# Kernel tuning notes

Hardware: AMD Instinct MI355X
Metric: run time of the kernel (lower is better)

Reference implementation:

```python
import jax, jax.numpy as jnp
import numpy as np

TOPK_RATIO = 0.2
DICE_WEIGHT = 0.5
SHAPE = (2, 1, 128, 192, 192)


def setup_inputs() -> dict:
    key = jax.random.key(0)
    k1, k2 = jax.random.split(key)
    logits = jax.random.normal(k1, SHAPE, dtype=jnp.float32)
    targets = jax.random.uniform(k2, SHAPE, dtype=jnp.float32)
    return {"logits": logits, "targets": targets}


def _bce_with_logits(x, t):
    # stable: max(x,0) - x*t + log(1+exp(-|x|))
    return jnp.maximum(x, 0.0) - x * t + jnp.log1p(jnp.exp(-jnp.abs(x)))


def reference(logits, targets):
    # --- TopK BCE ---
    flat_loss = _bce_with_logits(logits, targets).reshape(-1)
    n = flat_loss.shape[0]
    k_samples = max(1, int(n * TOPK_RATIO))
    topk_losses, _ = jax.lax.top_k(flat_loss, k_samples)
    bce = jnp.mean(topk_losses)

    # --- Soft Dice ---
    p = jax.nn.sigmoid(logits).reshape(-1)
    t = targets.reshape(-1)
    intersection = jnp.sum(p * t)
    union = jnp.sum(p) + jnp.sum(t)
    dice = (2.0 * intersection + 1e-06) / (union + 1e-06)
    dice_loss = 1.0 - dice

    return bce + DICE_WEIGHT * dice_loss
```

## Files before the change

### kernel.cpp

```cpp
#include <hip/hip_runtime.h>
#include <math.h>
#include <limits.h>

#define NB1 8192
#define NB2 4096
#define VEC 4

__device__ __forceinline__ void elem_f(float x, float t, float& l, float& p) {
    float e = __expf(-fabsf(x));
    l = fmaxf(x, 0.f) - x * t + __logf(1.f + e);
    float r = __builtin_amdgcn_rcpf(1.f + e);
    p = (x >= 0.f) ? r : e * r;
}

__global__ __launch_bounds__(256) void sample_kernel(
    const float4* __restrict__ x4, const float4* __restrict__ t4,
    unsigned* __restrict__ H1, int n4)
{
    __shared__ unsigned lh[NB1];
    for (int i = threadIdx.x; i < NB1; i += 256) lh[i] = 0u;
    __syncthreads();

    int nth = gridDim.x * 256;
    int tid = blockIdx.x * 256 + threadIdx.x;
    int S4 = n4 >> 4;
    int i0 = tid, i1 = tid + nth;

    float4 xa, ta, xb, tb;
    bool v0 = i0 < S4, v1 = i1 < S4;
    if (v0) {
        int f4 = ((i0 >> 6) << 10) + (i0 & 63);
        xa = x4[f4]; ta = t4[f4];
    }
    if (v1) {
        int f4 = ((i1 >> 6) << 10) + (i1 & 63);
        xb = x4[f4]; tb = t4[f4];
    }
    if (v0) {
        float xs[4] = {xa.x, xa.y, xa.z, xa.w};
        float ts[4] = {ta.x, ta.y, ta.z, ta.w};
        #pragma unroll
        for (int c = 0; c < 4; ++c) {
            float l, p; elem_f(xs[c], ts[c], l, p);
            atomicAdd(&lh[__float_as_uint(l) >> 19], 1u);
        }
    }
    if (v1) {
        float xs[4] = {xb.x, xb.y, xb.z, xb.w};
        float ts[4] = {tb.x, tb.y, tb.z, tb.w};
        #pragma unroll
        for (int c = 0; c < 4; ++c) {
            float l, p; elem_f(xs[c], ts[c], l, p);
            atomicAdd(&lh[__float_as_uint(l) >> 19], 1u);
        }
    }
    __syncthreads();
    for (int i = threadIdx.x; i < NB1; i += 256) {
        unsigned c = lh[i];
        if (c) atomicAdd(&H1[i], c);
    }
}

__global__ __launch_bounds__(256) void band_kernel(
    const unsigned* __restrict__ H1, float* __restrict__ band,
    long long ks, long long M)
{
    __shared__ unsigned lh[NB1];
    const uint4* hv = (const uint4*)H1;
    uint4* lv = (uint4*)lh;
    for (int i = threadIdx.x; i < NB1 / 4; i += 256) lv[i] = hv[i];
    __syncthreads();
    if (threadIdx.x >= 64) return;

    int lane = threadIdx.x;
    int base = lane << 7;
    unsigned long long chunk = 0;
    for (int j = 0; j < 128; ++j) chunk += lh[base + j];
    unsigned long long s = chunk;
    #pragma unroll
    for (int off = 1; off < 64; off <<= 1) {
        unsigned long long v = __shfl_down(s, off);
        if (lane + off < 64) s += v;
    }
    unsigned long long above = s - chunk;

    int my_bhi = INT_MAX, my_blo = -1;
    unsigned long long c = above;
    for (int j = 127; j >= 0; --j) {
        unsigned h = lh[base + j];
        if ((long long)(c + h) < ks - M) my_bhi = base + j;
        if ((long long)c > ks + M && my_blo < 0) my_blo = base + j;
        c += h;
    }
    #pragma unroll
    for (int off = 32; off; off >>= 1) {
        int a = __shfl_down(my_bhi, off); my_bhi = min(my_bhi, a);
        int b = __shfl_down(my_blo, off); my_blo = max(my_blo, b);
    }
    if (lane == 0) {
        int bhi = (my_bhi == INT_MAX) ? (NB1 - 1) : my_bhi;
        int blo = my_blo;
        float vhi = __uint_as_float((unsigned)bhi << 19);
        float vlo = (blo < 0) ? 0.f : __uint_as_float((unsigned)(blo + 1) << 19);
        if (!(vlo < vhi)) vlo = 0.f;
        band[0] = vlo;
        band[1] = vhi;
    }
}

__device__ __forceinline__ void process4(
    float4 xv, float4 tv, float vlo, float vhi, float scale,
    float& sp, float& spt, float& st, float& sgt, unsigned& cnt,
    unsigned* __restrict__ hist2)
{
    float xs[4] = {xv.x, xv.y, xv.z, xv.w};
    float ts[4] = {tv.x, tv.y, tv.z, tv.w};
    #pragma unroll
    for (int c = 0; c < 4; ++c) {
        float l, p;
        elem_f(xs[c], ts[c], l, p);
        sp += p; spt += p * ts[c]; st += ts[c];
        if (l >= vhi) { cnt++; sgt += l; }
        else if (l >= vlo) {
            int b = min((int)((l - vlo) * scale), NB2 - 1);
            atomicAdd(&hist2[b], 1u);
        }
    }
}

__global__ __launch_bounds__(256, 4) void main_kernel(
    const float4* __restrict__ x4, const float4* __restrict__ t4,
    const float* __restrict__ band, unsigned* __restrict__ hist2,
    float* __restrict__ q0, float* __restrict__ q1,
    float* __restrict__ q2, float* __restrict__ q3, unsigned* __restrict__ qc,
    const float* __restrict__ xg, const float* __restrict__ tg,
    int n, int n4)
{
    float vlo = band[0], vhi = band[1];
    float scale = (float)NB2 / (vhi - vlo);

    int base = blockIdx.x * (256 * VEC) + threadIdx.x;
    float sp = 0.f, spt = 0.f, st = 0.f, sgt = 0.f;
    unsigned cnt = 0;

    bool full = (blockIdx.x + 1) * (256 * VEC) <= n4;
    if (full) {
        float4 xv[VEC], tv[VEC];
        #pragma unroll
        for (int j = 0; j < VEC; ++j) xv[j] = x4[base + j * 256];
        #pragma unroll
        for (int j = 0; j < VEC; ++j) tv[j] = t4[base + j * 256];
        #pragma unroll
        for (int j = 0; j < VEC; ++j)
            process4(xv[j], tv[j], vlo, vhi, scale, sp, spt, st, sgt, cnt, hist2);
    } else {
        for (int j = 0; j < VEC; ++j) {
            int idx = base + j * 256;
            if (idx < n4)
                process4(x4[idx], t4[idx], vlo, vhi, scale, sp, spt, st, sgt, cnt, hist2);
        }
    }
    int tail0 = n4 << 2;
    if (blockIdx.x == 0 && threadIdx.x < (n - tail0)) {
        float x = xg[tail0 + threadIdx.x], t = tg[tail0 + threadIdx.x];
        float l, p;
        elem_f(x, t, l, p);
        sp += p; spt += p * t; st += t;
        if (l >= vhi) { cnt++; sgt += l; }
        else if (l >= vlo) {
            int b = min((int)((l - vlo) * scale), NB2 - 1);
            atomicAdd(&hist2[b], 1u);
        }
    }

    #pragma unroll
    for (int off = 32; off; off >>= 1) {
        sp  += __shfl_down(sp,  off);
        spt += __shfl_down(spt, off);
        st  += __shfl_down(st,  off);
        sgt += __shfl_down(sgt, off);
        cnt += __shfl_down(cnt, off);
    }
    __shared__ float    rs[4][4];
    __shared__ unsigned rc[4];
    int w = threadIdx.x >> 6;
    if ((threadIdx.x & 63) == 0) {
        rs[w][0] = sp; rs[w][1] = spt; rs[w][2] = st; rs[w][3] = sgt; rc[w] = cnt;
    }
    __syncthreads();
    if (threadIdx.x == 0) {
        float a0 = 0, a1 = 0, a2 = 0, a3 = 0;
        unsigned c = 0;
        #pragma unroll
        for (int i = 0; i < 4; ++i) {
            a0 += rs[i][0]; a1 += rs[i][1]; a2 += rs[i][2]; a3 += rs[i][3]; c += rc[i];
        }
        q0[blockIdx.x] = a0; q1[blockIdx.x] = a1; q2[blockIdx.x] = a2;
        q3[blockIdx.x] = a3; qc[blockIdx.x] = c;
    }
}

__global__ __launch_bounds__(1024) void final_kernel(
    const unsigned* __restrict__ hist2, const float* __restrict__ band,
    const float* __restrict__ q0, const float* __restrict__ q1,
    const float* __restrict__ q2, const float* __restrict__ q3,
    const unsigned* __restrict__ qc, int nblocks,
    float* __restrict__ out, long long k)
{
    __shared__ unsigned lh[NB2];
    __shared__ double red[16][5];
    __shared__ double fin[5];

    for (int i = threadIdx.x; i < NB2; i += 1024) lh[i] = hist2[i];

    double a0 = 0, a1 = 0, a2 = 0, a3 = 0, a4 = 0;
    for (int i = threadIdx.x; i < nblocks; i += 1024) {
        a0 += (double)q0[i]; a1 += (double)q1[i]; a2 += (double)q2[i];
        a3 += (double)q3[i]; a4 += (double)qc[i];
    }
    #pragma unroll
    for (int off = 32; off; off >>= 1) {
        a0 += __shfl_down(a0, off); a1 += __shfl_down(a1, off);
        a2 += __shfl_down(a2, off); a3 += __shfl_down(a3, off);
        a4 += __shfl_down(a4, off);
    }
    int w = threadIdx.x >> 6;
    if ((threadIdx.x & 63) == 0) {
        red[w][0] = a0; red[w][1] = a1; red[w][2] = a2; red[w][3] = a3; red[w][4] = a4;
    }
    __syncthreads();
    if (threadIdx.x == 0) {
        double f0 = 0, f1 = 0, f2 = 0, f3 = 0, f4 = 0;
        for (int i = 0; i < 16; ++i) {
            f0 += red[i][0]; f1 += red[i][1]; f2 += red[i][2];
            f3 += red[i][3]; f4 += red[i][4];
        }
        fin[0] = f0; fin[1] = f1; fin[2] = f2; fin[3] = f3; fin[4] = f4;
    }
    __syncthreads();
    if (threadIdx.x >= 64) return;

    int lane = threadIdx.x;
    double SP = fin[0], SPT = fin[1], ST = fin[2], SGT = fin[3];
    long long CNT = (long long)fin[4];

    double vlo = (double)band[0], vhi = (double)band[1];
    double binw = (vhi - vlo) / NB2;
    long long k2 = k - CNT;

    int base = lane << 6;
    unsigned long long cchunk = 0;
    double wchunk = 0.0;
    for (int j = 0; j < 64; ++j) {
        unsigned h = lh[base + j];
        cchunk += h;
        wchunk += (double)h * (vlo + (base + j + 0.5) * binw);
    }
    unsigned long long cs = cchunk;
    double wsum = wchunk;
    #pragma unroll
    for (int off = 1; off < 64; off <<= 1) {
        unsigned long long cv = __shfl_down(cs, off);
        double wv = __shfl_down(wsum, off);
        if (lane + off < 64) { cs += cv; wsum += wv; }
    }
    unsigned long long total = __shfl(cs, 0);
    double wtotal = __shfl(wsum, 0);

    double I = SPT, U = SP + ST;
    double dice_part = 0.5 * (1.0 - (2.0 * I + 1e-6) / (U + 1e-6));

    if (k2 <= 0) {
        if (lane == 0) out[0] = (float)(SGT / (double)k + dice_part);
        return;
    }
    if ((unsigned long long)k2 > total) {
        if (lane == 0) {
            double sum_top = SGT + wtotal + (double)(k2 - (long long)total) * vlo;
            out[0] = (float)(sum_top / (double)k + dice_part);
        }
        return;
    }
    unsigned long long c = cs - cchunk;
    double wacc = wsum - wchunk;
    for (int j = 63; j >= 0; --j) {
        unsigned h = lh[base + j];
        double val = vlo + (base + j + 0.5) * binw;
        if (c < (unsigned long long)k2 && (unsigned long long)k2 <= c + h) {
            double sum_top = SGT + wacc + (double)((long long)k2 - (long long)c) * val;
            out[0] = (float)(sum_top / (double)k + dice_part);
        }
        c += h;
        wacc += (double)h * val;
    }
}

extern "C" void kernel_launch(void* const* d_in, const int* in_sizes, int n_in,
                              void* d_out, int out_size, void* d_ws, size_t ws_size,
                              hipStream_t stream)
{
    const float* x = (const float*)d_in[0];
    const float* t = (const float*)d_in[1];
    float* out = (float*)d_out;
    int n = in_sizes[0];
    int n4 = n >> 2;
    long long k = (long long)((double)n * 0.2);
    if (k < 1) k = 1;

    long long S = (long long)(n4 >> 4) * 4;
    long long ks = (S > 0) ? (long long)((double)k * (double)S / (double)n) : 0;
    long long M = 4096;

    int tilesz = 256 * VEC;
    int grid = (n4 + tilesz - 1) / tilesz;
    if (grid < 1) grid = 1;

    int S4 = n4 >> 4;
    int sgrid = (S4 + 511) / 512;
    if (sgrid < 1) sgrid = 1;

    unsigned char* ws = (unsigned char*)d_ws;
    unsigned* H1    = (unsigned*)(ws);
    unsigned* hist2 = (unsigned*)(ws + 32768);
    float*    band  = (float*)(ws + 49152);
    size_t po = 50176;
    size_t pstride = (((size_t)grid * 4) + 255) & ~(size_t)255;
    float*    q0 = (float*)(ws + po);
    float*    q1 = (float*)(ws + po + pstride);
    float*    q2 = (float*)(ws + po + 2 * pstride);
    float*    q3 = (float*)(ws + po + 3 * pstride);
    unsigned* qc = (unsigned*)(ws + po + 4 * pstride);

    hipMemsetAsync(d_ws, 0, 49152, stream);

    sample_kernel<<<sgrid, 256, 0, stream>>>((const float4*)x, (const float4*)t, H1, n4);
    band_kernel<<<1, 256, 0, stream>>>(H1, band, ks, M);
    main_kernel<<<grid, 256, 0, stream>>>((const float4*)x, (const float4*)t,
                                          band, hist2, q0, q1, q2, q3, qc, x, t, n, n4);
    final_kernel<<<1, 1024, 0, stream>>>(hist2, band, q0, q1, q2, q3, qc, grid, out, k);
}
```

Before: 137.6 us.

## Fuse band and final stages into preceding kernels via last-block pattern

Replaces the four-kernel pipeline and memset with two kernels. The last block to finish, detected with a global atomic counter and threadfence, does the band selection and the final top-k and dice reduction. Histograms and counters move to __device__ globals that the last block resets for the next call. This removes two launches and a memset, but adds fence and atomic work to every block and a 16KB shared buffer to the main kernel, which may lower occupancy.

```diff
diff --git a/kernel.cpp b/kernel.cpp
--- a/kernel.cpp
+++ b/kernel.cpp
@@ -5,6 +5,12 @@
 #define NB1 8192
 #define NB2 4096
 #define VEC 4
+
+__device__ unsigned g_H1[NB1];
+__device__ unsigned g_hist2[NB2];
+__device__ float    g_band[2];
+__device__ unsigned g_done1 = 0;
+__device__ unsigned g_done2 = 0;
 
 __device__ __forceinline__ void elem_f(float x, float t, float& l, float& p) {
     float e = __expf(-fabsf(x));
@@ -13,11 +19,12 @@
     p = (x >= 0.f) ? r : e * r;
 }
 
-__global__ __launch_bounds__(256) void sample_kernel(
+__global__ __launch_bounds__(256) void sample_band_kernel(
     const float4* __restrict__ x4, const float4* __restrict__ t4,
-    unsigned* __restrict__ H1, int n4)
+    int n4, long long ks, long long M)
 {
     __shared__ unsigned lh[NB1];
+    __shared__ int is_last;
     for (int i = threadIdx.x; i < NB1; i += 256) lh[i] = 0u;
     __syncthreads();
 
@@ -57,54 +64,60 @@
     __syncthreads();
     for (int i = threadIdx.x; i < NB1; i += 256) {
         unsigned c = lh[i];
-        if (c) atomicAdd(&H1[i], c);
-    }
-}
-
-__global__ __launch_bounds__(256) void band_kernel(
-    const unsigned* __restrict__ H1, float* __restrict__ band,
-    long long ks, long long M)
-{
-    __shared__ unsigned lh[NB1];
-    const uint4* hv = (const uint4*)H1;
+        if (c) atomicAdd(&g_H1[i], c);
+    }
+    __syncthreads();
+
+    if (threadIdx.x == 0) {
+        __threadfence();
+        is_last = (atomicAdd(&g_done1, 1u) == (unsigned)(gridDim.x - 1));
+    }
+    __syncthreads();
+    if (!is_last) return;
+    __threadfence();
+
+    const uint4* hv = (const uint4*)g_H1;
     uint4* lv = (uint4*)lh;
     for (int i = threadIdx.x; i < NB1 / 4; i += 256) lv[i] = hv[i];
     __syncthreads();
-    if (threadIdx.x >= 64) return;
-
-    int lane = threadIdx.x;
-    int base = lane << 7;
-    unsigned long long chunk = 0;
-    for (int j = 0; j < 128; ++j) chunk += lh[base + j];
-    unsigned long long s = chunk;
-    #pragma unroll
-    for (int off = 1; off < 64; off <<= 1) {
-        unsigned long long v = __shfl_down(s, off);
-        if (lane + off < 64) s += v;
-    }
-    unsigned long long above = s - chunk;
-
-    int my_bhi = INT_MAX, my_blo = -1;
-    unsigned long long c = above;
-    for (int j = 127; j >= 0; --j) {
-        unsigned h = lh[base + j];
-        if ((long long)(c + h) < ks - M) my_bhi = base + j;
-        if ((long long)c > ks + M && my_blo < 0) my_blo = base + j;
-        c += h;
-    }
-    #pragma unroll
-    for (int off = 32; off; off >>= 1) {
-        int a = __shfl_down(my_bhi, off); my_bhi = min(my_bhi, a);
-        int b = __shfl_down(my_blo, off); my_blo = max(my_blo, b);
-    }
-    if (lane == 0) {
-        int bhi = (my_bhi == INT_MAX) ? (NB1 - 1) : my_bhi;
-        int blo = my_blo;
-        float vhi = __uint_as_float((unsigned)bhi << 19);
-        float vlo = (blo < 0) ? 0.f : __uint_as_float((unsigned)(blo + 1) << 19);
-        if (!(vlo < vhi)) vlo = 0.f;
-        band[0] = vlo;
-        band[1] = vhi;
+    for (int i = threadIdx.x; i < NB1; i += 256) g_H1[i] = 0u;
+    if (threadIdx.x == 0) g_done1 = 0u;
+
+    if (threadIdx.x < 64) {
+        int lane = threadIdx.x;
+        int base = lane << 7;
+        unsigned long long chunk = 0;
+        for (int j = 0; j < 128; ++j) chunk += lh[base + j];
+        unsigned long long s = chunk;
+        #pragma unroll
+        for (int off = 1; off < 64; off <<= 1) {
+            unsigned long long v = __shfl_down(s, off);
+            if (lane + off < 64) s += v;
+        }
+        unsigned long long above = s - chunk;
+
+        int my_bhi = INT_MAX, my_blo = -1;
+        unsigned long long c = above;
+        for (int j = 127; j >= 0; --j) {
+            unsigned h = lh[base + j];
+            if ((long long)(c + h) < ks - M) my_bhi = base + j;
+            if ((long long)c > ks + M && my_blo < 0) my_blo = base + j;
+            c += h;
+        }
+        #pragma unroll
+        for (int off = 32; off; off >>= 1) {
+            int a = __shfl_down(my_bhi, off); my_bhi = min(my_bhi, a);
+            int b = __shfl_down(my_blo, off); my_blo = max(my_blo, b);
+        }
+        if (lane == 0) {
+            int bhi = (my_bhi == INT_MAX) ? (NB1 - 1) : my_bhi;
+            int blo = my_blo;
+            float vhi = __uint_as_float((unsigned)bhi << 19);
+            float vlo = (blo < 0) ? 0.f : __uint_as_float((unsigned)(blo + 1) << 19);
+            if (!(vlo < vhi)) vlo = 0.f;
+            g_band[0] = vlo;
+            g_band[1] = vhi;
+        }
     }
 }
 
@@ -128,15 +141,21 @@
     }
 }
 
-__global__ __launch_bounds__(256, 4) void main_kernel(
+__global__ __launch_bounds__(256, 4) void main_final_kernel(
     const float4* __restrict__ x4, const float4* __restrict__ t4,
-    const float* __restrict__ band, unsigned* __restrict__ hist2,
     float* __restrict__ q0, float* __restrict__ q1,
     float* __restrict__ q2, float* __restrict__ q3, unsigned* __restrict__ qc,
     const float* __restrict__ xg, const float* __restrict__ tg,
-    int n, int n4)
+    int n, int n4, float* __restrict__ out, long long k)
 {
-    float vlo = band[0], vhi = band[1];
+    __shared__ float    rs[4][4];
+    __shared__ unsigned rc[4];
+    __shared__ int      is_last;
+    __shared__ unsigned lh2[NB2];
+    __shared__ double   red[4][5];
+    __shared__ double   fin[5];
+
+    float vlo = g_band[0], vhi = g_band[1];
     float scale = (float)NB2 / (vhi - vlo);
 
     int base = blockIdx.x * (256 * VEC) + threadIdx.x;
@@ -152,12 +171,12 @@
         for (int j = 0; j < VEC; ++j) tv[j] = t4[base + j * 256];
         #pragma unroll
         for (int j = 0; j < VEC; ++j)
-            process4(xv[j], tv[j], vlo, vhi, scale, sp, spt, st, sgt, cnt, hist2);
+            process4(xv[j], tv[j], vlo, vhi, scale, sp, spt, st, sgt, cnt, g_hist2);
     } else {
         for (int j = 0; j < VEC; ++j) {
             int idx = base + j * 256;
             if (idx < n4)
-                process4(x4[idx], t4[idx], vlo, vhi, scale, sp, spt, st, sgt, cnt, hist2);
+                process4(x4[idx], t4[idx], vlo, vhi, scale, sp, spt, st, sgt, cnt, g_hist2);
         }
     }
     int tail0 = n4 << 2;
@@ -169,7 +188,7 @@
         if (l >= vhi) { cnt++; sgt += l; }
         else if (l >= vlo) {
             int b = min((int)((l - vlo) * scale), NB2 - 1);
-            atomicAdd(&hist2[b], 1u);
+            atomicAdd(&g_hist2[b], 1u);
         }
     }
 
@@ -181,8 +200,6 @@
         sgt += __shfl_down(sgt, off);
         cnt += __shfl_down(cnt, off);
     }
-    __shared__ float    rs[4][4];
-    __shared__ unsigned rc[4];
     int w = threadIdx.x >> 6;
     if ((threadIdx.x & 63) == 0) {
         rs[w][0] = sp; rs[w][1] = spt; rs[w][2] = st; rs[w][3] = sgt; rc[w] = cnt;
@@ -197,24 +214,18 @@
         }
         q0[blockIdx.x] = a0; q1[blockIdx.x] = a1; q2[blockIdx.x] = a2;
         q3[blockIdx.x] = a3; qc[blockIdx.x] = c;
-    }
-}
-
-__global__ __launch_bounds__(1024) void final_kernel(
-    const unsigned* __restrict__ hist2, const float* __restrict__ band,
-    const float* __restrict__ q0, const float* __restrict__ q1,
-    const float* __restrict__ q2, const float* __restrict__ q3,
-    const unsigned* __restrict__ qc, int nblocks,
-    float* __restrict__ out, long long k)
-{
-    __shared__ unsigned lh[NB2];
-    __shared__ double red[16][5];
-    __shared__ double fin[5];
-
-    for (int i = threadIdx.x; i < NB2; i += 1024) lh[i] = hist2[i];
+        __threadfence();
+        is_last = (atomicAdd(&g_done2, 1u) == (unsigned)(gridDim.x - 1));
+    }
+    __syncthreads();
+    if (!is_last) return;
+    __threadfence();
+
+    int nblocks = gridDim.x;
+    for (int i = threadIdx.x; i < NB2; i += 256) lh2[i] = g_hist2[i];
 
     double a0 = 0, a1 = 0, a2 = 0, a3 = 0, a4 = 0;
-    for (int i = threadIdx.x; i < nblocks; i += 1024) {
+    for (int i = threadIdx.x; i < nblocks; i += 256) {
         a0 += (double)q0[i]; a1 += (double)q1[i]; a2 += (double)q2[i];
         a3 += (double)q3[i]; a4 += (double)qc[i];
     }
@@ -224,74 +235,75 @@
         a2 += __shfl_down(a2, off); a3 += __shfl_down(a3, off);
         a4 += __shfl_down(a4, off);
     }
-    int w = threadIdx.x >> 6;
+    int w2 = threadIdx.x >> 6;
     if ((threadIdx.x & 63) == 0) {
-        red[w][0] = a0; red[w][1] = a1; red[w][2] = a2; red[w][3] = a3; red[w][4] = a4;
+        red[w2][0] = a0; red[w2][1] = a1; red[w2][2] = a2; red[w2][3] = a3; red[w2][4] = a4;
     }
     __syncthreads();
     if (threadIdx.x == 0) {
         double f0 = 0, f1 = 0, f2 = 0, f3 = 0, f4 = 0;
-        for (int i = 0; i < 16; ++i) {
+        for (int i = 0; i < 4; ++i) {
             f0 += red[i][0]; f1 += red[i][1]; f2 += red[i][2];
             f3 += red[i][3]; f4 += red[i][4];
         }
         fin[0] = f0; fin[1] = f1; fin[2] = f2; fin[3] = f3; fin[4] = f4;
-    }
-    __syncthreads();
-    if (threadIdx.x >= 64) return;
-
-    int lane = threadIdx.x;
-    double SP = fin[0], SPT = fin[1], ST = fin[2], SGT = fin[3];
-    long long CNT = (long long)fin[4];
-
-    double vlo = (double)band[0], vhi = (double)band[1];
-    double binw = (vhi - vlo) / NB2;
-    long long k2 = k - CNT;
-
-    int base = lane << 6;
-    unsigned long long cchunk = 0;
-    double wchunk = 0.0;
-    for (int j = 0; j < 64; ++j) {
-        unsigned h = lh[base + j];
-        cchunk += h;
-        wchunk += (double)h * (vlo + (base + j + 0.5) * binw);
-    }
-    unsigned long long cs = cchunk;
-    double wsum = wchunk;
-    #pragma unroll
-    for (int off = 1; off < 64; off <<= 1) {
-        unsigned long long cv = __shfl_down(cs, off);
-        double wv = __shfl_down(wsum, off);
-        if (lane + off < 64) { cs += cv; wsum += wv; }
-    }
-    unsigned long long total = __shfl(cs, 0);
-    double wtotal = __shfl(wsum, 0);
-
-    double I = SPT, U = SP + ST;
-    double dice_part = 0.5 * (1.0 - (2.0 * I + 1e-6) / (U + 1e-6));
-
-    if (k2 <= 0) {
-        if (lane == 0) out[0] = (float)(SGT / (double)k + dice_part);
-        return;
-    }
-    if ((unsigned long long)k2 > total) {
-        if (lane == 0) {
-            double sum_top = SGT + wtotal + (double)(k2 - (long long)total) * vlo;
-            out[0] = (float)(sum_top / (double)k + dice_part);
-        }
-        return;
-    }
-    unsigned long long c = cs - cchunk;
-    double wacc = wsum - wchunk;
-    for (int j = 63; j >= 0; --j) {
-        unsigned h = lh[base + j];
-        double val = vlo + (base + j + 0.5) * binw;
-        if (c < (unsigned long long)k2 && (unsigned long long)k2 <= c + h) {
-            double sum_top = SGT + wacc + (double)((long long)k2 - (long long)c) * val;
-            out[0] = (float)(sum_top / (double)k + dice_part);
-        }
-        c += h;
-        wacc += (double)h * val;
+        g_done2 = 0u;
+    }
+    __syncthreads();
+    for (int i = threadIdx.x; i < NB2; i += 256) g_hist2[i] = 0u;
+
+    if (threadIdx.x < 64) {
+        int lane = threadIdx.x;
+        double SP = fin[0], SPT = fin[1], ST = fin[2], SGT = fin[3];
+        long long CNT = (long long)fin[4];
+
+        double dvlo = (double)vlo, dvhi = (double)vhi;
+        double binw = (dvhi - dvlo) / NB2;
+        long long k2 = k - CNT;
+
+        int base2 = lane << 6;
+        unsigned long long cchunk = 0;
+        double wchunk = 0.0;
+        for (int j = 0; j < 64; ++j) {
+            unsigned h = lh2[base2 + j];
+            cchunk += h;
+            wchunk += (double)h * (dvlo + (base2 + j + 0.5) * binw);
+        }
+        unsigned long long cs = cchunk;
+        double wsum = wchunk;
+        #pragma unroll
+        for (int off = 1; off < 64; off <<= 1) {
+            unsigned long long cv = __shfl_down(cs, off);
+            double wv = __shfl_down(wsum, off);
+            if (lane + off < 64) { cs += cv; wsum += wv; }
+        }
+        unsigned long long total = __shfl(cs, 0);
+        double wtotal = __shfl(wsum, 0);
+
+        double I = SPT, U = SP + ST;
+        double dice_part = 0.5 * (1.0 - (2.0 * I + 1e-6) / (U + 1e-6));
+
+        if (k2 <= 0) {
+            if (lane == 0) out[0] = (float)(SGT / (double)k + dice_part);
+        } else if ((unsigned long long)k2 > total) {
+            if (lane == 0) {
+                double sum_top = SGT + wtotal + (double)(k2 - (long long)total) * dvlo;
+                out[0] = (float)(sum_top / (double)k + dice_part);
+            }
+        } else {
+            unsigned long long c = cs - cchunk;
+            double wacc = wsum - wchunk;
+            for (int j = 63; j >= 0; --j) {
+                unsigned h = lh2[base2 + j];
+                double val = dvlo + (base2 + j + 0.5) * binw;
+                if (c < (unsigned long long)k2 && (unsigned long long)k2 <= c + h) {
+                    double sum_top = SGT + wacc + (double)((long long)k2 - (long long)c) * val;
+                    out[0] = (float)(sum_top / (double)k + dice_part);
+                }
+                c += h;
+                wacc += (double)h * val;
+            }
+        }
     }
 }
 
@@ -320,22 +332,15 @@
     if (sgrid < 1) sgrid = 1;
 
     unsigned char* ws = (unsigned char*)d_ws;
-    unsigned* H1    = (unsigned*)(ws);
-    unsigned* hist2 = (unsigned*)(ws + 32768);
-    float*    band  = (float*)(ws + 49152);
-    size_t po = 50176;
     size_t pstride = (((size_t)grid * 4) + 255) & ~(size_t)255;
-    float*    q0 = (float*)(ws + po);
-    float*    q1 = (float*)(ws + po + pstride);
-    float*    q2 = (float*)(ws + po + 2 * pstride);
-    float*    q3 = (float*)(ws + po + 3 * pstride);
-    unsigned* qc = (unsigned*)(ws + po + 4 * pstride);
-
-    hipMemsetAsync(d_ws, 0, 49152, stream);
-
-    sample_kernel<<<sgrid, 256, 0, stream>>>((const float4*)x, (const float4*)t, H1, n4);
-    band_kernel<<<1, 256, 0, stream>>>(H1, band, ks, M);
-    main_kernel<<<grid, 256, 0, stream>>>((const float4*)x, (const float4*)t,
-                                          band, hist2, q0, q1, q2, q3, qc, x, t, n, n4);
-    final_kernel<<<1, 1024, 0, stream>>>(hist2, band, q0, q1, q2, q3, qc, grid, out, k);
-}
+    float*    q0 = (float*)(ws);
+    float*    q1 = (float*)(ws + pstride);
+    float*    q2 = (float*)(ws + 2 * pstride);
+    float*    q3 = (float*)(ws + 3 * pstride);
+    unsigned* qc = (unsigned*)(ws + 4 * pstride);
+
+    sample_band_kernel<<<sgrid, 256, 0, stream>>>((const float4*)x, (const float4*)t,
+                                                  n4, ks, M);
+    main_final_kernel<<<grid, 256, 0, stream>>>((const float4*)x, (const float4*)t,
+                                                q0, q1, q2, q3, qc, x, t, n, n4, out, k);
+}
```

New measurement: 202.4 us. 47.0% more time.
